# Kernel tuning notes

Hardware: AMD Instinct MI355X
Metric: run time of the kernel (lower is better)

## Reference

```python
import jax, jax.numpy as jnp
import numpy as np

X_DIM, Z_DIM, N_HEIGHT = 256, 256, 32
EPS = 1e-5  # BatchNorm1d eps

def _bn(x, g, b):
    # BatchNorm1d in training mode: batch statistics over the point axis
    m = x.mean(0)
    v = x.var(0)
    return (x - m) * jax.lax.rsqrt(v + EPS) * g + b

def setup_inputs() -> dict:
    key = jax.random.key(0)
    ks = jax.random.split(key, 16)
    B, N, F = 2, 120000, 3
    inp = {
        'pt_fea': jax.random.normal(ks[0], (B, N, F), jnp.float32),
        'grid_ind': jax.random.randint(ks[1], (B, N, 2), 0, 256, dtype=jnp.int32).astype(jnp.int64),
        'occupancy': (jax.random.uniform(ks[2], (B, 1, X_DIM, N_HEIGHT, Z_DIM)) < 0.1).astype(jnp.float32),
    }
    dims = [(3, 64), (64, 128), (128, 256), (256, 512)]
    for i, (di, do) in enumerate(dims):
        inp[f'W{i+1}'] = jax.random.normal(ks[3 + i], (di, do), jnp.float32) * 0.02
        inp[f'b{i+1}'] = jnp.zeros((do,), jnp.float32)
    for i, d in enumerate([3, 64, 128, 256]):
        inp[f'g{i}'] = jnp.ones((d,), jnp.float32)
        inp[f'be{i}'] = jnp.zeros((d,), jnp.float32)
    inp['Wc'] = jax.random.normal(ks[10], (512, 32), jnp.float32) * 0.02
    inp['bc'] = jnp.zeros((32,), jnp.float32)
    return inp

def reference(pt_fea, occupancy, W1, b1, W2, b2, W3, b3, W4, b4,
              g0, be0, g1, be1, g2, be2, g3, be3, Wc, bc, grid_ind):
    B, N, F = pt_fea.shape
    feats = pt_fea.reshape(B * N, F)                          # cat over batch
    # PointNet per-point MLP: BN -> (Linear -> BN -> ReLU) x3 -> Linear
    h = _bn(feats, g0, be0)
    h = jax.nn.relu(_bn(h @ W1 + b1, g1, be1))
    h = jax.nn.relu(_bn(h @ W2 + b2, g2, be2))
    h = jax.nn.relu(_bn(h @ W3 + b3, g3, be3))
    h = h @ W4 + b4                                           # [B*N, 512]

    # linear segment id per (batch, x, z) cell; equivalent to unique+scatter_max
    gi = grid_ind.reshape(B * N, 2).astype(jnp.int32)
    batch_idx = jnp.repeat(jnp.arange(B, dtype=jnp.int32), N)
    seg = batch_idx * (X_DIM * Z_DIM) + gi[:, 0] * Z_DIM + gi[:, 1]
    n_cells = B * X_DIM * Z_DIM

    pooled = jax.ops.segment_max(h, seg, num_segments=n_cells)          # [cells, 512]
    cnt = jax.ops.segment_sum(jnp.ones((B * N,), h.dtype), seg, num_segments=n_cells)
    occ_mask = (cnt > 0)[:, None]
    pooled = jnp.where(occ_mask, pooled, 0.0)                           # kill -inf empties

    # feature compression on occupied cells only; empty cells stay exactly 0
    comp = jax.nn.relu(pooled @ Wc + bc)
    comp = jnp.where(occ_mask, comp, 0.0)                               # [cells, 32]

    bev = comp.reshape(B, X_DIM, Z_DIM, -1).transpose(0, 3, 1, 2)       # [B, 32, X, Z]
    # MaxPool2d(k=3, stride=1, pad=1); -inf padding matches torch's implicit -inf pad
    bev = jax.lax.reduce_window(bev, -jnp.inf, jax.lax.max,
                                (1, 1, 3, 3), (1, 1, 1, 1), 'SAME')

    occu = occupancy[:, 0].transpose(0, 2, 1, 3)                        # [B, H, X, Z]
    out = jnp.concatenate([occu, bev], axis=1)                          # [B, H+32, X, Z]
    return out
```

## Files before the change

### kernel.cpp

```cpp
#include <hip/hip_runtime.h>
#include <hip/hip_bf16.h>

#define EPSN 1e-5f

typedef __bf16 bf16x8 __attribute__((ext_vector_type(8)));
typedef float f32x4 __attribute__((ext_vector_type(4)));

__device__ __forceinline__ unsigned encf(float f) {
  unsigned u = __float_as_uint(f);
  return (u & 0x80000000u) ? ~u : (u | 0x80000000u);
}
__device__ __forceinline__ float decf(unsigned u) {
  return (u & 0x80000000u) ? __uint_as_float(u ^ 0x80000000u) : __uint_as_float(~u);
}

__global__ __launch_bounds__(256) void stats_feats(const float* __restrict__ pt, int n,
                                                   float* __restrict__ sums) {
  float a0 = 0, a1 = 0, a2 = 0, q0 = 0, q1 = 0, q2 = 0;
  for (int p = blockIdx.x * 256 + threadIdx.x; p < n; p += gridDim.x * 256) {
    float v0 = pt[3 * p], v1 = pt[3 * p + 1], v2 = pt[3 * p + 2];
    a0 += v0; a1 += v1; a2 += v2;
    q0 += v0 * v0; q1 += v1 * v1; q2 += v2 * v2;
  }
  __shared__ float red[4][6];
  float vals[6] = {a0, a1, a2, q0, q1, q2};
  int lane = threadIdx.x & 63, wv = threadIdx.x >> 6;
#pragma unroll
  for (int k = 0; k < 6; k++) {
    float v = vals[k];
#pragma unroll
    for (int o = 32; o; o >>= 1) v += __shfl_down(v, o, 64);
    if (lane == 0) red[wv][k] = v;
  }
  __syncthreads();
  if (threadIdx.x < 6) {
    float v = red[0][threadIdx.x] + red[1][threadIdx.x] + red[2][threadIdx.x] + red[3][threadIdx.x];
    atomicAdd(&sums[threadIdx.x], v);
  }
}

__global__ void bn_prep(const float* __restrict__ sums, int C, float invN,
                        const float* __restrict__ g, const float* __restrict__ be,
                        float* __restrict__ sc, float* __restrict__ sh) {
  int c = threadIdx.x;
  if (c < C) {
    float m = sums[c] * invN;
    float v = fmaxf(sums[C + c] * invN - m * m, 0.f);
    float s = g[c] * rsqrtf(v + EPSN);
    sc[c] = s;
    sh[c] = be[c] - m * s;
  }
}

__global__ __launch_bounds__(256) void wconv(const float* __restrict__ W,
                                             __hip_bfloat16* __restrict__ Wt, int K, int C) {
  int idx = blockIdx.x * 256 + threadIdx.x;
  if (idx >= K * C) return;
  int k = idx / C, c = idx - k * C;
  Wt[(size_t)c * K + k] = __float2bfloat16(W[idx]);
}

__global__ __launch_bounds__(256) void gemm1_stats(const float* __restrict__ pt,
                                                   const float* __restrict__ W,
                                                   const float* __restrict__ bias,
                                                   const float* __restrict__ scsh,
                                                   __hip_bfloat16* __restrict__ Y,
                                                   int n, float* __restrict__ sums) {
  const int c = threadIdx.x & 63;
  const float w0 = W[c], w1 = W[64 + c], w2 = W[128 + c], bb = bias[c];
  const float s0 = scsh[0], s1 = scsh[1], s2 = scsh[2];
  const float h0 = scsh[4], h1 = scsh[5], h2 = scsh[6];
  float s = 0.f, q = 0.f;
  const int total = n * 64;
  for (int idx = blockIdx.x * 256 + threadIdx.x; idx < total; idx += gridDim.x * 256) {
    int p = idx >> 6;
    float x0 = s0 * pt[3 * p]     + h0;
    float x1 = s1 * pt[3 * p + 1] + h1;
    float x2 = s2 * pt[3 * p + 2] + h2;
    float y = bb + x0 * w0 + x1 * w1 + x2 * w2;
    Y[idx] = __float2bfloat16(y);
    s += y; q += y * y;
  }
  __shared__ float sred[4][64], qred[4][64];
  int wv = threadIdx.x >> 6;
  sred[wv][c] = s; qred[wv][c] = q;
  __syncthreads();
  if (threadIdx.x < 64) {
    float S = sred[0][c] + sred[1][c] + sred[2][c] + sred[3][c];
    float Q = qred[0][c] + qred[1][c] + qred[2][c] + qred[3][c];
    atomicAdd(&sums[c], S);
    atomicAdd(&sums[64 + c], Q);
  }
}

template <int K>
__global__ __launch_bounds__(256) void gemm_mfma(
    const __hip_bfloat16* __restrict__ Yin, const __hip_bfloat16* __restrict__ Wt,
    const float* __restrict__ bias, const float* __restrict__ sc, const float* __restrict__ sh,
    __hip_bfloat16* __restrict__ Yout, int C, float* __restrict__ sums, int nrows) {
  constexpr int KS = 64, LDA = 72, LDO = 80;
  __shared__ __align__(16) __hip_bfloat16 hA[128 * LDO];
  __shared__ float sredArr[128], qredArr[128];
  const int t = threadIdx.x;
  const int lane = t & 63, wv = t >> 6;
  const int mh = (wv >> 1) * 64, nh = (wv & 1) * 64;
  const int lm = lane & 15, lq = lane >> 4;
  const int p0 = blockIdx.x * 128;
  const int cb0 = blockIdx.y * 128;

  f32x4 acc[4][4];
#pragma unroll
  for (int i = 0; i < 4; i++)
#pragma unroll
    for (int j = 0; j < 4; j++) acc[i][j] = {0.f, 0.f, 0.f, 0.f};

  for (int k0 = 0; k0 < K; k0 += KS) {
    __syncthreads();
#pragma unroll
    for (int it = 0; it < 4; it++) {
      int idx = it * 256 + t;
      int row = idx >> 3;
      int c8 = (idx & 7) * 8;
      int gp = p0 + row;
      __hip_bfloat16 h8[8];
      if (gp < nrows) {
        uint4 raw = *(const uint4*)(Yin + (size_t)gp * K + k0 + c8);
        const __hip_bfloat16* pr = (const __hip_bfloat16*)&raw;
#pragma unroll
        for (int j = 0; j < 8; j++) {
          float v = sc[k0 + c8 + j] * __bfloat162float(pr[j]) + sh[k0 + c8 + j];
          h8[j] = __float2bfloat16(fmaxf(v, 0.f));
        }
      } else {
#pragma unroll
        for (int j = 0; j < 8; j++) h8[j] = __float2bfloat16(0.f);
      }
      *(uint4*)&hA[row * LDA + c8] = *(const uint4*)h8;
    }
    __syncthreads();
#pragma unroll
    for (int kk = 0; kk < KS; kk += 32) {
      bf16x8 a[4], b[4];
#pragma unroll
      for (int i = 0; i < 4; i++)
        a[i] = *(const bf16x8*)&hA[(mh + i * 16 + lm) * LDA + kk + lq * 8];
#pragma unroll
      for (int j = 0; j < 4; j++)
        b[j] = *(const bf16x8*)(const void*)(Wt + (size_t)(cb0 + nh + j * 16 + lm) * K + k0 + kk + lq * 8);
#pragma unroll
      for (int i = 0; i < 4; i++)
#pragma unroll
        for (int j = 0; j < 4; j++)
          acc[i][j] = __builtin_amdgcn_mfma_f32_16x16x32_bf16(a[i], b[j], acc[i][j], 0, 0, 0);
    }
  }

#pragma unroll
  for (int j = 0; j < 4; j++) {
    float bb = bias[cb0 + nh + j * 16 + lm];
#pragma unroll
    for (int i = 0; i < 4; i++)
#pragma unroll
      for (int r = 0; r < 4; r++) acc[i][j][r] += bb;
  }

  __syncthreads();
  if (t < 128) { sredArr[t] = 0.f; qredArr[t] = 0.f; }
  __syncthreads();

#pragma unroll
  for (int j = 0; j < 4; j++) {
    float s = 0.f, q = 0.f;
#pragma unroll
    for (int i = 0; i < 4; i++)
#pragma unroll
      for (int r = 0; r < 4; r++) {
        int grow = p0 + mh + i * 16 + lq * 4 + r;
        if (grow < nrows) { float v = acc[i][j][r]; s += v; q += v * v; }
      }
    s += __shfl_xor(s, 16); s += __shfl_xor(s, 32);
    q += __shfl_xor(q, 16); q += __shfl_xor(q, 32);
    if (lq == 0) {
      atomicAdd(&sredArr[nh + j * 16 + lm], s);
      atomicAdd(&qredArr[nh + j * 16 + lm], q);
    }
  }

  for (int half = 0; half < 2; half++) {
    __syncthreads();
    if ((wv & 1) == half) {
#pragma unroll
      for (int j = 0; j < 4; j++)
#pragma unroll
        for (int i = 0; i < 4; i++)
#pragma unroll
          for (int r = 0; r < 4; r++)
            hA[(mh + i * 16 + lq * 4 + r) * LDO + j * 16 + lm] = __float2bfloat16(acc[i][j][r]);
    }
    __syncthreads();
    int row = t >> 1, seg = t & 1;
    if (p0 + row < nrows) {
      const uint4* src = (const uint4*)&hA[row * LDO + seg * 32];
      uint4* dst = (uint4*)(Yout + (size_t)(p0 + row) * C + cb0 + half * 64 + seg * 32);
      dst[0] = src[0]; dst[1] = src[1]; dst[2] = src[2]; dst[3] = src[3];
    }
  }

  if (t < 128) {
    atomicAdd(&sums[cb0 + t], sredArr[t]);
    atomicAdd(&sums[C + cb0 + t], qredArr[t]);
  }
}

__global__ __launch_bounds__(256) void hist_kernel(const int* __restrict__ gi, int perB,
                                                   unsigned* __restrict__ hist) {
  int b = blockIdx.y;
  int p = blockIdx.x * 256 + threadIdx.x;
  if (p < perB) {
    int gp = b * perB + p;
    int c = (gi[2 * gp] & 255) * 256 + (gi[2 * gp + 1] & 255);
    atomicAdd(&hist[b * 65536 + c], 1u);
  }
}
__global__ __launch_bounds__(256) void scan1(const unsigned* __restrict__ hist,
                                             unsigned* __restrict__ cursor,
                                             unsigned* __restrict__ bSums) {
  __shared__ unsigned s[256];
  int b = blockIdx.y;
  int t = threadIdx.x, i = b * 65536 + blockIdx.x * 256 + t;
  unsigned v = hist[i]; s[t] = v; __syncthreads();
  for (int off = 1; off < 256; off <<= 1) {
    unsigned x = (t >= off) ? s[t - off] : 0u; __syncthreads();
    s[t] += x; __syncthreads();
  }
  cursor[i] = s[t] - v;
  if (t == 255) bSums[b * 256 + blockIdx.x] = s[255];
}
__global__ void scan2(unsigned* __restrict__ bSums) {
  __shared__ unsigned s[256];
  int t = threadIdx.x, i = blockIdx.x * 256 + t;
  unsigned v = bSums[i]; s[t] = v; __syncthreads();
  for (int off = 1; off < 256; off <<= 1) {
    unsigned x = (t >= off) ? s[t - off] : 0u; __syncthreads();
    s[t] += x; __syncthreads();
  }
  bSums[i] = s[t] - v;
}
__global__ __launch_bounds__(256) void mk_starts(const unsigned* __restrict__ cursor,
                                                 const unsigned* __restrict__ bSums,
                                                 unsigned* __restrict__ starts, int perB) {
  int b = blockIdx.y;
  int i = blockIdx.x * 256 + threadIdx.x;
  starts[b * 65537 + i] = cursor[b * 65536 + i] + bSums[b * 256 + (i >> 8)];
  if (i == 0) starts[b * 65537 + 65536] = (unsigned)perB;
}
__global__ __launch_bounds__(256) void scatter_kernel(const int* __restrict__ gi, int perB,
                                                      unsigned* __restrict__ cursor,
                                                      const unsigned* __restrict__ bSums,
                                                      unsigned* __restrict__ sorted,
                                                      unsigned* __restrict__ cells) {
  int b = blockIdx.y;
  int p = blockIdx.x * 256 + threadIdx.x;
  if (p < perB) {
    int gp = b * perB + p;
    int c = (gi[2 * gp] & 255) * 256 + (gi[2 * gp + 1] & 255);
    unsigned pos = atomicAdd(&cursor[b * 65536 + c], 1u) + bSums[b * 256 + (c >> 8)];
    if (pos < (unsigned)perB) {
      sorted[b * perB + pos] = (unsigned)p;
      cells[b * perB + pos] = (unsigned)c;
    }
  }
}

__global__ __launch_bounds__(256, 2) void pool_compress(
    const __hip_bfloat16* __restrict__ Y3, const __hip_bfloat16* __restrict__ Wt4,
    const float* __restrict__ b4, const float* __restrict__ sc, const float* __restrict__ sh,
    const __hip_bfloat16* __restrict__ WcT, const float* __restrict__ bc,
    const unsigned* __restrict__ sortedIdx, const unsigned* __restrict__ sortedCell,
    const unsigned* __restrict__ startsAll, float* __restrict__ comp, int perB) {
  constexpr int K = 256, KS = 64, LDA = 72, MLW = 132;
  __shared__ __align__(16) __hip_bfloat16 hA[128 * LDA];
  __shared__ __align__(16) unsigned maxLds[64 * MLW];
  __shared__ unsigned char slotRow[256];
  __shared__ int rowIdxLds[256];
  const int t = threadIdx.x;
  const int lane = t & 63, wv = t >> 6;
  const int lm = lane & 15, lq = lane >> 4;
  const int mh = (wv >> 1) * 64, nh = (wv & 1) * 64;
  const int batch = blockIdx.y;
  const unsigned* starts = startsAll + batch * 65537;
  const int c0 = blockIdx.x * 64;
  const int r0 = (int)starts[c0];
  int n = (int)starts[c0 + 64] - r0;
  if (n > 256) n = 256;
  if (n < 0) n = 0;
  const int nrg = (n + 127) >> 7;

  for (int i = t; i < n; i += 256) {
    rowIdxLds[i] = (int)sortedIdx[batch * perB + r0 + i] + batch * perB;
    slotRow[i] = (unsigned char)((sortedCell[batch * perB + r0 + i] - c0) & 63);
  }

  f32x4 accC[2];
  accC[0] = {0.f, 0.f, 0.f, 0.f};
  accC[1] = {0.f, 0.f, 0.f, 0.f};

  for (int cc = 0; cc < 4; cc++) {
    __syncthreads();
    for (int i = t; i < 64 * MLW; i += 256) maxLds[i] = 0u;
    for (int rg = 0; rg < nrg; rg++) {
      const int rbase = rg * 128;
      f32x4 acc[4][4];
#pragma unroll
      for (int i = 0; i < 4; i++)
#pragma unroll
        for (int j = 0; j < 4; j++) acc[i][j] = {0.f, 0.f, 0.f, 0.f};
      for (int k0 = 0; k0 < K; k0 += KS) {
        __syncthreads();
#pragma unroll
        for (int it = 0; it < 4; it++) {
          int idx = it * 256 + t;
          int row = idx >> 3;
          int c8 = (idx & 7) * 8;
          int gr = rbase + row;
          __hip_bfloat16 h8[8];
          if (gr < n) {
            uint4 raw = *(const uint4*)(Y3 + (size_t)rowIdxLds[gr] * K + k0 + c8);
            const __hip_bfloat16* pr = (const __hip_bfloat16*)&raw;
#pragma unroll
            for (int j = 0; j < 8; j++) {
              float v = sc[k0 + c8 + j] * __bfloat162float(pr[j]) + sh[k0 + c8 + j];
              h8[j] = __float2bfloat16(fmaxf(v, 0.f));
            }
          } else {
#pragma unroll
            for (int j = 0; j < 8; j++) h8[j] = __float2bfloat16(0.f);
          }
          *(uint4*)&hA[row * LDA + c8] = *(const uint4*)h8;
        }
        __syncthreads();
#pragma unroll
        for (int kk = 0; kk < KS; kk += 32) {
          bf16x8 a[4], b[4];
#pragma unroll
          for (int i = 0; i < 4; i++)
            a[i] = *(const bf16x8*)&hA[(mh + i * 16 + lm) * LDA + kk + lq * 8];
#pragma unroll
          for (int j = 0; j < 4; j++)
            b[j] = *(const bf16x8*)(const void*)(Wt4 + (size_t)(cc * 128 + nh + j * 16 + lm) * K + k0 + kk + lq * 8);
#pragma unroll
          for (int i = 0; i < 4; i++)
#pragma unroll
            for (int j = 0; j < 4; j++)
              acc[i][j] = __builtin_amdgcn_mfma_f32_16x16x32_bf16(a[i], b[j], acc[i][j], 0, 0, 0);
        }
      }
#pragma unroll
      for (int j = 0; j < 4; j++) {
        int colq = nh + j * 16 + lm;
#pragma unroll
        for (int i = 0; i < 4; i++) {
#pragma unroll
          for (int r = 0; r < 4; r++) {
            int lrow = rbase + mh + i * 16 + lq * 4 + r;
            if (lrow < n)
              atomicMax(&maxLds[(int)slotRow[lrow] * MLW + colq], encf(acc[i][j][r]));
          }
        }
      }
    }
    __syncthreads();
#pragma unroll
    for (int ks = 0; ks < 4; ks++) {
      int koff = ks * 32 + lq * 8;
      uint4 m0 = *(const uint4*)&maxLds[(wv * 16 + lm) * MLW + koff];
      uint4 m1 = *(const uint4*)&maxLds[(wv * 16 + lm) * MLW + koff + 4];
      unsigned mu[8] = {m0.x, m0.y, m0.z, m0.w, m1.x, m1.y, m1.z, m1.w};
      __hip_bfloat16 af[8];
#pragma unroll
      for (int j = 0; j < 8; j++)
        af[j] = __float2bfloat16(decf(mu[j]) + b4[cc * 128 + koff + j]);
      bf16x8 a = *(const bf16x8*)af;
#pragma unroll
      for (int jn = 0; jn < 2; jn++) {
        bf16x8 b = *(const bf16x8*)(const void*)(WcT + (size_t)(jn * 16 + lm) * 512 + cc * 128 + koff);
        accC[jn] = __builtin_amdgcn_mfma_f32_16x16x32_bf16(a, b, accC[jn], 0, 0, 0);
      }
    }
  }
#pragma unroll
  for (int jn = 0; jn < 2; jn++) {
    float bb = bc[jn * 16 + lm];
#pragma unroll
    for (int r = 0; r < 4; r++) {
      int cell = c0 + wv * 16 + lq * 4 + r;
      int occ = starts[cell + 1] > starts[cell];
      float v = occ ? fmaxf(accC[jn][r] + bb, 0.f) : 0.f;
      comp[((size_t)batch * 65536 + cell) * 32 + jn * 16 + lm] = v;
    }
  }
}

__global__ __launch_bounds__(256) void maxpool_write(const float* __restrict__ comp,
                                                     float* __restrict__ out) {
  __shared__ float tile[32][65];
  int bid = blockIdx.x;
  int z0 = (bid & 3) * 64, x = (bid >> 2) & 255, b = bid >> 10;
  int f = threadIdx.x & 31, zs = threadIdx.x >> 5;
  for (int zi = 0; zi < 8; zi++) {
    int z = z0 + zi * 8 + zs;
    float m = -3.402823466e38f;
    for (int dx = -1; dx <= 1; dx++) {
      int xx = x + dx;
      if (xx < 0 || xx > 255) continue;
      for (int dz = -1; dz <= 1; dz++) {
        int zz = z + dz;
        if (zz < 0 || zz > 255) continue;
        m = fmaxf(m, comp[(size_t)((b << 16) + (xx << 8) + zz) * 32 + f]);
      }
    }
    tile[f][zi * 8 + zs] = m;
  }
  __syncthreads();
  int f2 = threadIdx.x >> 3, seg = threadIdx.x & 7;
  float* dst = out + ((size_t)(b * 64 + 32 + f2) * 256 + x) * 256 + z0 + seg * 8;
#pragma unroll
  for (int u = 0; u < 8; u++) dst[u] = tile[f2][seg * 8 + u];
}

__global__ __launch_bounds__(256) void occu_write(const float* __restrict__ occ,
                                                  float* __restrict__ out) {
  int idx = blockIdx.x * 256 + threadIdx.x;
  int z = idx & 255, x = (idx >> 8) & 255, hh = (idx >> 16) & 31, b = idx >> 21;
  out[((size_t)(b * 64 + hh) * 256 + x) * 256 + z] =
      occ[((size_t)((b * 256 + x) * 32 + hh)) * 256 + z];
}

extern "C" void kernel_launch(void* const* d_in, const int* in_sizes, int n_in,
                              void* d_out, int out_size, void* d_ws, size_t ws_size,
                              hipStream_t stream) {
  const float* pt_fea   = (const float*)d_in[0];
  const int*   grid_ind = (const int*)d_in[1];
  const float* occup    = (const float*)d_in[2];
  const float* W1 = (const float*)d_in[3];  const float* b1 = (const float*)d_in[4];
  const float* W2 = (const float*)d_in[5];  const float* b2 = (const float*)d_in[6];
  const float* W3 = (const float*)d_in[7];  const float* b3 = (const float*)d_in[8];
  const float* W4 = (const float*)d_in[9];  const float* b4 = (const float*)d_in[10];
  const float* g0 = (const float*)d_in[11]; const float* be0 = (const float*)d_in[12];
  const float* g1 = (const float*)d_in[13]; const float* be1 = (const float*)d_in[14];
  const float* g2 = (const float*)d_in[15]; const float* be2 = (const float*)d_in[16];
  const float* g3 = (const float*)d_in[17]; const float* be3 = (const float*)d_in[18];
  const float* Wc = (const float*)d_in[19]; const float* bc = (const float*)d_in[20];
  float* out = (float*)d_out;

  const int nPts = in_sizes[0] / 3;
  const int perB = nPts / 2;
  const float invN = 1.f / (float)nPts;

  char* ws = (char*)d_ws;
  float* stats = (float*)ws;
  float* scsh  = (float*)(ws + 4096);
  float* sums0 = stats;        float* sums1 = stats + 16;
  float* sums2 = stats + 160;  float* sums3 = stats + 416;
  float* sc0 = scsh;
  float* sc1 = scsh + 16;   float* sh1 = scsh + 80;
  float* sc2 = scsh + 144;  float* sh2 = scsh + 272;
  float* sc3 = scsh + 400;  float* sh3 = scsh + 656;
  __hip_bfloat16* Wt2 = (__hip_bfloat16*)(ws + 8192);
  __hip_bfloat16* Wt3 = (__hip_bfloat16*)(ws + 24576);
  __hip_bfloat16* Wt4 = (__hip_bfloat16*)(ws + 90112);
  __hip_bfloat16* WcT = (__hip_bfloat16*)(ws + 352256);
  char* S0 = ws + 385024;
  __hip_bfloat16* Y1 = (__hip_bfloat16*)S0;
  __hip_bfloat16* Y2 = (__hip_bfloat16*)(S0 + 30720000ll);
  __hip_bfloat16* Y3 = (__hip_bfloat16*)(S0 + 92160000ll);
  float* comp       = (float*)S0;
  char* sortBase    = S0 + 16777216ll;
  unsigned* hist    = (unsigned*)sortBase;
  unsigned* cursor  = hist + 2 * 65536;
  unsigned* bSums   = cursor + 2 * 65536;
  unsigned* startsA = bSums + 1024;
  unsigned* sorted  = startsA + 131080;
  unsigned* cells   = sorted + 2 * perB;

  hipMemsetAsync(stats, 0, 4096, stream);

  wconv<<<(64 * 128 + 255) / 256, 256, 0, stream>>>(W2, Wt2, 64, 128);
  wconv<<<(128 * 256 + 255) / 256, 256, 0, stream>>>(W3, Wt3, 128, 256);
  wconv<<<(256 * 512 + 255) / 256, 256, 0, stream>>>(W4, Wt4, 256, 512);
  wconv<<<(512 * 32 + 255) / 256, 256, 0, stream>>>(Wc, WcT, 512, 32);

  stats_feats<<<256, 256, 0, stream>>>(pt_fea, nPts, sums0);
  bn_prep<<<1, 256, 0, stream>>>(sums0, 3, invN, g0, be0, sc0, scsh + 4);

  gemm1_stats<<<512, 256, 0, stream>>>(pt_fea, W1, b1, scsh, Y1, nPts, sums1);
  bn_prep<<<1, 256, 0, stream>>>(sums1, 64, invN, g1, be1, sc1, sh1);

  gemm_mfma<64><<<dim3(nPts / 128, 1), 256, 0, stream>>>(Y1, Wt2, b2, sc1, sh1, Y2, 128, sums2, nPts);
  bn_prep<<<1, 256, 0, stream>>>(sums2, 128, invN, g2, be2, sc2, sh2);

  gemm_mfma<128><<<dim3(nPts / 128, 2), 256, 0, stream>>>(Y2, Wt3, b3, sc2, sh2, Y3, 256, sums3, nPts);
  bn_prep<<<1, 256, 0, stream>>>(sums3, 256, invN, g3, be3, sc3, sh3);

  hipMemsetAsync(hist, 0, 2 * 65536 * 4, stream);
  const int pgrid = (perB + 255) / 256;
  hist_kernel<<<dim3(pgrid, 2), 256, 0, stream>>>(grid_ind, perB, hist);
  scan1<<<dim3(256, 2), 256, 0, stream>>>(hist, cursor, bSums);
  scan2<<<2, 256, 0, stream>>>(bSums);
  mk_starts<<<dim3(256, 2), 256, 0, stream>>>(cursor, bSums, startsA, perB);
  scatter_kernel<<<dim3(pgrid, 2), 256, 0, stream>>>(grid_ind, perB, cursor, bSums, sorted, cells);

  pool_compress<<<dim3(1024, 2), 256, 0, stream>>>(
      Y3, Wt4, b4, sc3, sh3, WcT, bc, sorted, cells, startsA, comp, perB);

  maxpool_write<<<2048, 256, 0, stream>>>(comp, out);
  occu_write<<<16384, 256, 0, stream>>>(occup, out);
}
```

Before: 779.6 us.

## Shrink pool_compress cell tile and reuse gathered rows across two column chunks

pool_compress now takes 40 cells per block instead of 64, so the sorted point rows fit in a single 128-row tile (capped at 128 rows). Each gathered and BN-normalised A tile is reused for 256 output columns at once instead of 128, halving the number of Y3 gather and normalisation passes. The b4 bias is added before the segment max rather than after, which gives the same result. In exchange, accumulator register use doubles, only three of four waves do the compression MFMAs, and the 128-row tile holds fewer cells, so more padded rows go through the MFMAs.

```diff
diff --git a/kernel.cpp b/kernel.cpp
--- a/kernel.cpp
+++ b/kernel.cpp
@@ -278,125 +278,144 @@
     const __hip_bfloat16* __restrict__ WcT, const float* __restrict__ bc,
     const unsigned* __restrict__ sortedIdx, const unsigned* __restrict__ sortedCell,
     const unsigned* __restrict__ startsAll, float* __restrict__ comp, int perB) {
-  constexpr int K = 256, KS = 64, LDA = 72, MLW = 132;
+  constexpr int K = 256, KS = 64, LDA = 72, MLW = 129, NC = 40;
   __shared__ __align__(16) __hip_bfloat16 hA[128 * LDA];
-  __shared__ __align__(16) unsigned maxLds[64 * MLW];
-  __shared__ unsigned char slotRow[256];
-  __shared__ int rowIdxLds[256];
+  __shared__ __align__(16) unsigned maxLds[48 * MLW];
+  __shared__ unsigned char slotRow[128];
+  __shared__ int rowIdxLds[128];
   const int t = threadIdx.x;
   const int lane = t & 63, wv = t >> 6;
   const int lm = lane & 15, lq = lane >> 4;
   const int mh = (wv >> 1) * 64, nh = (wv & 1) * 64;
   const int batch = blockIdx.y;
   const unsigned* starts = startsAll + batch * 65537;
-  const int c0 = blockIdx.x * 64;
+  const int c0 = blockIdx.x * NC;
+  const int cEnd = min(c0 + NC, 65536);
   const int r0 = (int)starts[c0];
-  int n = (int)starts[c0 + 64] - r0;
-  if (n > 256) n = 256;
+  int n = (int)starts[cEnd] - r0;
+  if (n > 128) n = 128;
   if (n < 0) n = 0;
-  const int nrg = (n + 127) >> 7;
-
-  for (int i = t; i < n; i += 256) {
-    rowIdxLds[i] = (int)sortedIdx[batch * perB + r0 + i] + batch * perB;
-    slotRow[i] = (unsigned char)((sortedCell[batch * perB + r0 + i] - c0) & 63);
+
+  if (t < 128) {
+    if (t < n) {
+      rowIdxLds[t] = (int)sortedIdx[batch * perB + r0 + t] + batch * perB;
+      slotRow[t] = (unsigned char)((sortedCell[batch * perB + r0 + t] - c0) % NC);
+    } else {
+      rowIdxLds[t] = 0;
+      slotRow[t] = 0;
+    }
   }
 
   f32x4 accC[2];
   accC[0] = {0.f, 0.f, 0.f, 0.f};
   accC[1] = {0.f, 0.f, 0.f, 0.f};
 
-  for (int cc = 0; cc < 4; cc++) {
-    __syncthreads();
-    for (int i = t; i < 64 * MLW; i += 256) maxLds[i] = 0u;
-    for (int rg = 0; rg < nrg; rg++) {
-      const int rbase = rg * 128;
-      f32x4 acc[4][4];
+  for (int half = 0; half < 2; half++) {
+    f32x4 acc[2][4][4];
+#pragma unroll
+    for (int s2 = 0; s2 < 2; s2++)
 #pragma unroll
       for (int i = 0; i < 4; i++)
 #pragma unroll
-        for (int j = 0; j < 4; j++) acc[i][j] = {0.f, 0.f, 0.f, 0.f};
-      for (int k0 = 0; k0 < K; k0 += KS) {
-        __syncthreads();
-#pragma unroll
-        for (int it = 0; it < 4; it++) {
-          int idx = it * 256 + t;
-          int row = idx >> 3;
-          int c8 = (idx & 7) * 8;
-          int gr = rbase + row;
-          __hip_bfloat16 h8[8];
-          if (gr < n) {
-            uint4 raw = *(const uint4*)(Y3 + (size_t)rowIdxLds[gr] * K + k0 + c8);
-            const __hip_bfloat16* pr = (const __hip_bfloat16*)&raw;
-#pragma unroll
-            for (int j = 0; j < 8; j++) {
-              float v = sc[k0 + c8 + j] * __bfloat162float(pr[j]) + sh[k0 + c8 + j];
-              h8[j] = __float2bfloat16(fmaxf(v, 0.f));
-            }
-          } else {
-#pragma unroll
-            for (int j = 0; j < 8; j++) h8[j] = __float2bfloat16(0.f);
+        for (int j = 0; j < 4; j++) acc[s2][i][j] = {0.f, 0.f, 0.f, 0.f};
+
+    for (int k0 = 0; k0 < K; k0 += KS) {
+      __syncthreads();
+#pragma unroll
+      for (int it = 0; it < 4; it++) {
+        int idx = it * 256 + t;
+        int row = idx >> 3;
+        int c8 = (idx & 7) * 8;
+        __hip_bfloat16 h8[8];
+        if (row < n) {
+          uint4 raw = *(const uint4*)(Y3 + (size_t)rowIdxLds[row] * K + k0 + c8);
+          const __hip_bfloat16* pr = (const __hip_bfloat16*)&raw;
+#pragma unroll
+          for (int j = 0; j < 8; j++) {
+            float v = sc[k0 + c8 + j] * __bfloat162float(pr[j]) + sh[k0 + c8 + j];
+            h8[j] = __float2bfloat16(fmaxf(v, 0.f));
           }
-          *(uint4*)&hA[row * LDA + c8] = *(const uint4*)h8;
+        } else {
+#pragma unroll
+          for (int j = 0; j < 8; j++) h8[j] = __float2bfloat16(0.f);
         }
-        __syncthreads();
-#pragma unroll
-        for (int kk = 0; kk < KS; kk += 32) {
-          bf16x8 a[4], b[4];
+        *(uint4*)&hA[row * LDA + c8] = *(const uint4*)h8;
+      }
+      __syncthreads();
+#pragma unroll
+      for (int kk = 0; kk < KS; kk += 32) {
+        bf16x8 a[4];
+#pragma unroll
+        for (int i = 0; i < 4; i++)
+          a[i] = *(const bf16x8*)&hA[(mh + i * 16 + lm) * LDA + kk + lq * 8];
+#pragma unroll
+        for (int s2 = 0; s2 < 2; s2++) {
+          bf16x8 b[4];
+#pragma unroll
+          for (int j = 0; j < 4; j++)
+            b[j] = *(const bf16x8*)(const void*)(Wt4 + (size_t)(half * 256 + s2 * 128 + nh + j * 16 + lm) * K + k0 + kk + lq * 8);
 #pragma unroll
           for (int i = 0; i < 4; i++)
-            a[i] = *(const bf16x8*)&hA[(mh + i * 16 + lm) * LDA + kk + lq * 8];
-#pragma unroll
-          for (int j = 0; j < 4; j++)
-            b[j] = *(const bf16x8*)(const void*)(Wt4 + (size_t)(cc * 128 + nh + j * 16 + lm) * K + k0 + kk + lq * 8);
-#pragma unroll
-          for (int i = 0; i < 4; i++)
 #pragma unroll
             for (int j = 0; j < 4; j++)
-              acc[i][j] = __builtin_amdgcn_mfma_f32_16x16x32_bf16(a[i], b[j], acc[i][j], 0, 0, 0);
+              acc[s2][i][j] = __builtin_amdgcn_mfma_f32_16x16x32_bf16(a[i], b[j], acc[s2][i][j], 0, 0, 0);
         }
       }
+    }
+
+    for (int s2 = 0; s2 < 2; s2++) {
+      const int cc = half * 2 + s2;
+      __syncthreads();
+      for (int i = t; i < 48 * MLW; i += 256) maxLds[i] = 0u;
+      __syncthreads();
 #pragma unroll
       for (int j = 0; j < 4; j++) {
         int colq = nh + j * 16 + lm;
+        float bb = b4[cc * 128 + colq];
 #pragma unroll
         for (int i = 0; i < 4; i++) {
 #pragma unroll
           for (int r = 0; r < 4; r++) {
-            int lrow = rbase + mh + i * 16 + lq * 4 + r;
+            int lrow = mh + i * 16 + lq * 4 + r;
             if (lrow < n)
-              atomicMax(&maxLds[(int)slotRow[lrow] * MLW + colq], encf(acc[i][j][r]));
+              atomicMax(&maxLds[(int)slotRow[lrow] * MLW + colq], encf(acc[s2][i][j][r] + bb));
           }
         }
       }
-    }
-    __syncthreads();
-#pragma unroll
-    for (int ks = 0; ks < 4; ks++) {
-      int koff = ks * 32 + lq * 8;
-      uint4 m0 = *(const uint4*)&maxLds[(wv * 16 + lm) * MLW + koff];
-      uint4 m1 = *(const uint4*)&maxLds[(wv * 16 + lm) * MLW + koff + 4];
-      unsigned mu[8] = {m0.x, m0.y, m0.z, m0.w, m1.x, m1.y, m1.z, m1.w};
-      __hip_bfloat16 af[8];
-#pragma unroll
-      for (int j = 0; j < 8; j++)
-        af[j] = __float2bfloat16(decf(mu[j]) + b4[cc * 128 + koff + j]);
-      bf16x8 a = *(const bf16x8*)af;
-#pragma unroll
-      for (int jn = 0; jn < 2; jn++) {
-        bf16x8 b = *(const bf16x8*)(const void*)(WcT + (size_t)(jn * 16 + lm) * 512 + cc * 128 + koff);
-        accC[jn] = __builtin_amdgcn_mfma_f32_16x16x32_bf16(a, b, accC[jn], 0, 0, 0);
-      }
-    }
-  }
-#pragma unroll
-  for (int jn = 0; jn < 2; jn++) {
-    float bb = bc[jn * 16 + lm];
-#pragma unroll
-    for (int r = 0; r < 4; r++) {
-      int cell = c0 + wv * 16 + lq * 4 + r;
-      int occ = starts[cell + 1] > starts[cell];
-      float v = occ ? fmaxf(accC[jn][r] + bb, 0.f) : 0.f;
-      comp[((size_t)batch * 65536 + cell) * 32 + jn * 16 + lm] = v;
+      __syncthreads();
+      if (wv < 3) {
+#pragma unroll
+        for (int ks = 0; ks < 4; ks++) {
+          int koff = ks * 32 + lq * 8;
+          uint4 m0 = *(const uint4*)&maxLds[(wv * 16 + lm) * MLW + koff];
+          uint4 m1 = *(const uint4*)&maxLds[(wv * 16 + lm) * MLW + koff + 4];
+          unsigned mu[8] = {m0.x, m0.y, m0.z, m0.w, m1.x, m1.y, m1.z, m1.w};
+          __hip_bfloat16 af[8];
+#pragma unroll
+          for (int j = 0; j < 8; j++) af[j] = __float2bfloat16(decf(mu[j]));
+          bf16x8 a = *(const bf16x8*)af;
+#pragma unroll
+          for (int jn = 0; jn < 2; jn++) {
+            bf16x8 b = *(const bf16x8*)(const void*)(WcT + (size_t)(jn * 16 + lm) * 512 + cc * 128 + koff);
+            accC[jn] = __builtin_amdgcn_mfma_f32_16x16x32_bf16(a, b, accC[jn], 0, 0, 0);
+          }
+        }
+      }
+    }
+  }
+  if (wv < 3) {
+#pragma unroll
+    for (int jn = 0; jn < 2; jn++) {
+      float bb = bc[jn * 16 + lm];
+#pragma unroll
+      for (int r = 0; r < 4; r++) {
+        int cell = c0 + wv * 16 + lq * 4 + r;
+        if (cell < cEnd) {
+          int occ = starts[cell + 1] > starts[cell];
+          float v = occ ? fmaxf(accC[jn][r] + bb, 0.f) : 0.f;
+          comp[((size_t)batch * 65536 + cell) * 32 + jn * 16 + lm] = v;
+        }
+      }
     }
   }
 }
@@ -510,7 +529,7 @@
   mk_starts<<<dim3(256, 2), 256, 0, stream>>>(cursor, bSums, startsA, perB);
   scatter_kernel<<<dim3(pgrid, 2), 256, 0, stream>>>(grid_ind, perB, cursor, bSums, sorted, cells);
 
-  pool_compress<<<dim3(1024, 2), 256, 0, stream>>>(
+  pool_compress<<<dim3((65536 + 39) / 40, 2), 256, 0, stream>>>(
       Y3, Wt4, b4, sc3, sh3, WcT, bc, sorted, cells, startsA, comp, perB);
 
   maxpool_write<<<2048, 256, 0, stream>>>(comp, out);
```

Result: slower. 1.648 ms (+111.3%).
